# Kernel optimization log

Measured on AMD Instinct MI355X. Metric: run time of the kernel, lower is better.

The kernel has to match this reference:

```python
import jax, jax.numpy as jnp
import numpy as np

D_MODEL = 1024
N_HEAD = 16
HEAD_DIM = D_MODEL // N_HEAD
BS, SEQ = 4, 2048
NEG_INF = -1e9


def setup_inputs() -> dict:
    key = jax.random.key(0)
    ks = jax.random.split(key, 10)
    X = jax.random.normal(ks[0], (BS, SEQ, D_MODEL), dtype=jnp.float32)
    kpm = jax.random.randint(ks[1], (BS, SEQ), 0, 2, dtype=jnp.int32)
    kpm = kpm.at[:, 0].set(0)  # guarantee at least one attendable key per batch
    scale = 1.0 / np.sqrt(D_MODEL)
    WQ = jax.random.normal(ks[2], (D_MODEL, D_MODEL), dtype=jnp.float32) * scale
    bQ = jnp.zeros((D_MODEL,), dtype=jnp.float32)
    WK = jax.random.normal(ks[3], (D_MODEL, D_MODEL), dtype=jnp.float32) * scale
    bK = jnp.zeros((D_MODEL,), dtype=jnp.float32)
    WV = jax.random.normal(ks[4], (D_MODEL, D_MODEL), dtype=jnp.float32) * scale
    bV = jnp.zeros((D_MODEL,), dtype=jnp.float32)
    WO = jax.random.normal(ks[5], (D_MODEL, D_MODEL), dtype=jnp.float32) * scale
    bO = jnp.zeros((D_MODEL,), dtype=jnp.float32)
    return {"X": X, "key_padding_mask": kpm, "WQ": WQ, "bQ": bQ,
            "WK": WK, "bK": bK, "WV": WV, "bV": bV, "WO": WO, "bO": bO}


def reference(X, key_padding_mask, WQ, bQ, WK, bK, WV, bV, WO, bO):
    bs, L, _ = X.shape
    # separate Q/K/V linear projections (torch Linear: x @ W.T + b)
    Q = X @ WQ.T + bQ
    K = X @ WK.T + bK
    V = X @ WV.T + bV
    # split heads: (bs, L, H, Dh) -> (bs, H, L, Dh)
    Q = Q.reshape(bs, L, N_HEAD, HEAD_DIM).transpose(0, 2, 1, 3)
    K = K.reshape(bs, L, N_HEAD, HEAD_DIM).transpose(0, 2, 1, 3)
    V = V.reshape(bs, L, N_HEAD, HEAD_DIM).transpose(0, 2, 1, 3)
    # scaled dot-product attention
    scores = jnp.einsum('bhqd,bhkd->bhqk', Q, K) / jnp.sqrt(
        jnp.asarray(HEAD_DIM, dtype=Q.dtype))
    # key padding mask: non-zero => ignore that key
    mask = (key_padding_mask != 0)[:, None, None, :]  # (bs,1,1,L)
    scores = jnp.where(mask, NEG_INF, scores)
    attn = jax.nn.softmax(scores, axis=-1)
    out = jnp.einsum('bhqk,bhkd->bhqd', attn, V)
    # merge heads
    out = out.transpose(0, 2, 1, 3).reshape(bs, L, D_MODEL)
    return out @ WO.T + bO
```

## Files before the change

### kernel.cpp

```cpp
#include <hip/hip_runtime.h>
#include <stdint.h>

#define BS_   4
#define SEQ_  2048
#define DM_   1024
#define NH_   16
#define DH_   64
#define MTOK_ (BS_*SEQ_)

typedef __attribute__((ext_vector_type(8))) short bf16x8;
typedef __attribute__((ext_vector_type(4))) float f32x4;

#define SA_ 0.18033688011112042f
#define SHIFT_ 16.0f

__device__ __forceinline__ unsigned short f2bf(float f) {
    union { float f; uint32_t u; } v; v.f = f;
    uint32_t r = v.u + 0x7fffu + ((v.u >> 16) & 1u);
    return (unsigned short)(r >> 16);
}

__device__ __forceinline__ float fexp2(float x) {
#if __has_builtin(__builtin_amdgcn_exp2f)
    return __builtin_amdgcn_exp2f(x);
#else
    return __expf(x * 0.69314718055994531f);
#endif
}

__device__ __forceinline__ uint32_t cvt_pk_bf16(float lo, float hi) {
    uint32_t r;
    asm("v_cvt_pk_bf16_f32 %0, %1, %2" : "=v"(r) : "v"(lo), "v"(hi));
    return r;
}

__device__ __forceinline__ void gload_lds16(const void* g, void* l) {
    __builtin_amdgcn_global_load_lds(
        (const __attribute__((address_space(1))) void*)g,
        (__attribute__((address_space(3))) void*)l, 16, 0, 0);
}

__global__ void cvt_kernel(const float* __restrict__ src,
                           unsigned short* __restrict__ dst, int n) {
    int i = (blockIdx.x * blockDim.x + threadIdx.x) * 4;
    const int stride = gridDim.x * blockDim.x * 4;
    for (; i < n; i += stride) {
        float4 v = *(const float4*)(src + i);
        ushort4 o;
        o.x = f2bf(v.x); o.y = f2bf(v.y); o.z = f2bf(v.z); o.w = f2bf(v.w);
        *(ushort4*)(dst + i) = o;
    }
}

__global__ void cvt4_kernel(const float* __restrict__ s0, const float* __restrict__ s1,
                            const float* __restrict__ s2, const float* __restrict__ s3,
                            unsigned short* __restrict__ dst) {
    const int i = (blockIdx.x * blockDim.x + threadIdx.x) * 4;
    const int mat = i >> 20;
    const int off = i & ((1 << 20) - 1);
    const float* s = (mat == 0) ? s0 : (mat == 1) ? s1 : (mat == 2) ? s2 : s3;
    float4 v = *(const float4*)(s + off);
    ushort4 o;
    o.x = f2bf(v.x); o.y = f2bf(v.y); o.z = f2bf(v.z); o.w = f2bf(v.w);
    *(ushort4*)(dst + i) = o;
}

template<int MODE>
__global__ __launch_bounds__(256) void gemm_bt(
    const unsigned short* __restrict__ A,
    const unsigned short* __restrict__ B,
    int Ndim, int Kdim,
    const float* __restrict__ bias0,
    const float* __restrict__ bias1,
    const float* __restrict__ bias2,
    unsigned short* __restrict__ Qo,
    unsigned short* __restrict__ Ko,
    unsigned short* __restrict__ Vt,
    float* __restrict__ Co)
{
    __shared__ unsigned short As[128 * 32];
    __shared__ unsigned short Bs[128 * 32];

    const int t    = threadIdx.x;
    const int lane = t & 63;
    const int w    = t >> 6;
    const int wr   = w >> 1, wc = w & 1;
    const int g    = lane >> 4, li = lane & 15;

    const int ntile = Ndim >> 7;
    const int per   = gridDim.x >> 3;
    const int sw    = (blockIdx.x & 7) * per + (blockIdx.x >> 3);
    const int tm = sw / ntile;
    const int tn = sw % ntile;

    const unsigned short* Ab = A + (size_t)tm * 128 * Kdim;
    const unsigned short* Bb = B + (size_t)tn * 128 * Kdim;

    f32x4 acc[4][4];
    const f32x4 zero = {0.f, 0.f, 0.f, 0.f};
    #pragma unroll
    for (int i = 0; i < 4; ++i)
        #pragma unroll
        for (int j = 0; j < 4; ++j)
            acc[i][j] = zero;

    const int s0 = t, s1 = t + 256;
    const int r0 = s0 >> 2, c0 = (s0 & 3) << 3;
    const int r1 = s1 >> 2, c1 = (s1 & 3) << 3;

    for (int k0 = 0; k0 < Kdim; k0 += 32) {
        gload_lds16(Ab + (size_t)r0 * Kdim + k0 + c0, (char*)As + s0 * 16);
        gload_lds16(Ab + (size_t)r1 * Kdim + k0 + c1, (char*)As + s1 * 16);
        gload_lds16(Bb + (size_t)r0 * Kdim + k0 + c0, (char*)Bs + s0 * 16);
        gload_lds16(Bb + (size_t)r1 * Kdim + k0 + c1, (char*)Bs + s1 * 16);
        __syncthreads();

        bf16x8 a[4], b[4];
        #pragma unroll
        for (int mi = 0; mi < 4; ++mi)
            a[mi] = *(const bf16x8*)&As[(wr * 64 + mi * 16 + li) * 32 + g * 8];
        #pragma unroll
        for (int ni = 0; ni < 4; ++ni)
            b[ni] = *(const bf16x8*)&Bs[(wc * 64 + ni * 16 + li) * 32 + g * 8];

        #pragma unroll
        for (int mi = 0; mi < 4; ++mi)
            #pragma unroll
            for (int ni = 0; ni < 4; ++ni)
                acc[mi][ni] = __builtin_amdgcn_mfma_f32_16x16x32_bf16(
                    a[mi], b[ni], acc[mi][ni], 0, 0, 0);
        __syncthreads();
    }

    if constexpr (MODE == 0) {
        #pragma unroll
        for (int mi = 0; mi < 4; ++mi) {
            const int gm0 = tm * 128 + wr * 64 + mi * 16 + g * 4;
            const int bb  = gm0 >> 11;
            const int l0  = gm0 & (SEQ_ - 1);
            #pragma unroll
            for (int ni = 0; ni < 4; ++ni) {
                const int gn  = tn * 128 + wc * 64 + ni * 16 + li;
                const int mat = gn >> 10;
                const int c   = gn & (DM_ - 1);
                const int hh  = c >> 6;
                const int dd  = c & (DH_ - 1);
                const float bias = (mat == 0 ? bias0 : (mat == 1 ? bias1 : bias2))[c];
                const f32x4 v = acc[mi][ni];
                if (mat == 2) {
                    ushort4 o;
                    o.x = f2bf(v[0] + bias);
                    o.y = f2bf(v[1] + bias);
                    o.z = f2bf(v[2] + bias);
                    o.w = f2bf(v[3] + bias);
                    *(ushort4*)&Vt[((size_t)(bb * NH_ + hh) * DH_ + dd) * SEQ_ + l0] = o;
                } else {
                    unsigned short* dst = (mat == 0) ? Qo : Ko;
                    #pragma unroll
                    for (int r = 0; r < 4; ++r)
                        dst[((size_t)(bb * NH_ + hh) * SEQ_ + l0 + r) * DH_ + dd] =
                            f2bf(v[r] + bias);
                }
            }
        }
    } else {
        #pragma unroll
        for (int mi = 0; mi < 4; ++mi) {
            const int gm0 = tm * 128 + wr * 64 + mi * 16 + g * 4;
            #pragma unroll
            for (int ni = 0; ni < 4; ++ni) {
                const int gn = tn * 128 + wc * 64 + ni * 16 + li;
                const float bias = bias0[gn];
                #pragma unroll
                for (int r = 0; r < 4; ++r)
                    Co[(size_t)(gm0 + r) * Ndim + gn] = acc[mi][ni][r] + bias;
            }
        }
    }
}

#define KPAD 72

__global__ __launch_bounds__(256) void attn_kernel(
    const unsigned short* __restrict__ Q,
    const unsigned short* __restrict__ K,
    const unsigned short* __restrict__ Vt,
    const int* __restrict__ kpm,
    unsigned short* __restrict__ Oo)
{
    __shared__ unsigned short Ks[64 * KPAD];
    __shared__ unsigned short Vs[64 * KPAD];
    __shared__ float maskLds[64];

    const int t    = threadIdx.x;
    const int lane = t & 63;
    const int w    = t >> 6;
    const int g    = lane >> 4, li = lane & 15;

    const int bh = blockIdx.x >> 4;
    const int qt = blockIdx.x & 15;
    const int b  = bh >> 4;
    const int h  = bh & 15;
    const int q0 = qt * 128 + w * 32;

    bf16x8 qf[2][2];
    #pragma unroll
    for (int qi = 0; qi < 2; ++qi)
        #pragma unroll
        for (int kk = 0; kk < 2; ++kk)
            qf[qi][kk] = *(const bf16x8*)&Q[((size_t)bh * SEQ_ + q0 + qi * 16 + li) * DH_
                                            + kk * 32 + g * 8];

    f32x4 Oacc[2][4];
    const f32x4 zero = {0.f, 0.f, 0.f, 0.f};
    #pragma unroll
    for (int qi = 0; qi < 2; ++qi)
        #pragma unroll
        for (int di = 0; di < 4; ++di)
            Oacc[qi][di] = zero;

    float lrun[2] = {0.f, 0.f};

    const int sr = t >> 3;
    const int sc = (t & 7) * 8;

    bf16x8 kreg0, kreg1, vreg0, vreg1;
    float mreg = 0.f;

    auto load_tile = [&](int kv) {
        kreg0 = *(const bf16x8*)&K[((size_t)bh * SEQ_ + kv + sr) * DH_ + sc];
        kreg1 = *(const bf16x8*)&K[((size_t)bh * SEQ_ + kv + sr + 32) * DH_ + sc];
        vreg0 = *(const bf16x8*)&Vt[((size_t)bh * DH_ + sr) * SEQ_ + kv + sc];
        vreg1 = *(const bf16x8*)&Vt[((size_t)bh * DH_ + sr + 32) * SEQ_ + kv + sc];
        if (t < 64) mreg = (kpm[b * SEQ_ + kv + t] ? -1e9f : 0.0f) - SHIFT_;
    };
    auto store_tile = [&]() {
        *(bf16x8*)&Ks[sr * KPAD + sc] = kreg0;
        *(bf16x8*)&Ks[(sr + 32) * KPAD + sc] = kreg1;
        *(bf16x8*)&Vs[sr * KPAD + sc] = vreg0;
        *(bf16x8*)&Vs[(sr + 32) * KPAD + sc] = vreg1;
        if (t < 64) maskLds[t] = mreg;
    };

    load_tile(0);
    store_tile();

    for (int kv = 0; kv < SEQ_; kv += 64) {
        __syncthreads();
        const bool more = (kv + 64) < SEQ_;
        if (more) load_tile(kv + 64);

        float4 mk[4];
        #pragma unroll
        for (int ni = 0; ni < 4; ++ni)
            mk[ni] = *(const float4*)&maskLds[ni * 16 + g * 4];

        f32x4 sacc[2][4];
        #pragma unroll
        for (int qi = 0; qi < 2; ++qi)
            #pragma unroll
            for (int ni = 0; ni < 4; ++ni)
                sacc[qi][ni] = zero;
        __builtin_amdgcn_s_setprio(1);
        #pragma unroll
        for (int ni = 0; ni < 4; ++ni) {
            #pragma unroll
            for (int kk = 0; kk < 2; ++kk) {
                bf16x8 kb = *(const bf16x8*)&Ks[(ni * 16 + li) * KPAD + kk * 32 + g * 8];
                sacc[0][ni] = __builtin_amdgcn_mfma_f32_16x16x32_bf16(
                    kb, qf[0][kk], sacc[0][ni], 0, 0, 0);
                sacc[1][ni] = __builtin_amdgcn_mfma_f32_16x16x32_bf16(
                    kb, qf[1][kk], sacc[1][ni], 0, 0, 0);
            }
        }
        __builtin_amdgcn_s_setprio(0);

        #pragma unroll
        for (int qi = 0; qi < 2; ++qi) {
            float rs = 0.f;
            #pragma unroll
            for (int ni = 0; ni < 4; ++ni) {
                #pragma unroll
                for (int r = 0; r < 4; ++r) {
                    const float mval = (r == 0) ? mk[ni].x : (r == 1) ? mk[ni].y
                                      : (r == 2) ? mk[ni].z : mk[ni].w;
                    const float p = fexp2(fmaf(sacc[qi][ni][r], SA_, mval));
                    sacc[qi][ni][r] = p;
                    rs += p;
                }
            }
            lrun[qi] += rs;
        }

        bf16x8 pa[2][2];
        #pragma unroll
        for (int qi = 0; qi < 2; ++qi)
            #pragma unroll
            for (int kk = 0; kk < 2; ++kk) {
                union { bf16x8 v; uint32_t w4[4]; } u;
                u.w4[0] = cvt_pk_bf16(sacc[qi][2 * kk][0],     sacc[qi][2 * kk][1]);
                u.w4[1] = cvt_pk_bf16(sacc[qi][2 * kk][2],     sacc[qi][2 * kk][3]);
                u.w4[2] = cvt_pk_bf16(sacc[qi][2 * kk + 1][0], sacc[qi][2 * kk + 1][1]);
                u.w4[3] = cvt_pk_bf16(sacc[qi][2 * kk + 1][2], sacc[qi][2 * kk + 1][3]);
                pa[qi][kk] = u.v;
            }

        __builtin_amdgcn_s_setprio(1);
        #pragma unroll
        for (int di = 0; di < 4; ++di) {
            #pragma unroll
            for (int kk = 0; kk < 2; ++kk) {
                union { bf16x8 v; ushort4 h[2]; } uv;
                uv.h[0] = *(const ushort4*)&Vs[(di * 16 + li) * KPAD + kk * 32 + g * 4];
                uv.h[1] = *(const ushort4*)&Vs[(di * 16 + li) * KPAD + kk * 32 + 16 + g * 4];
                Oacc[0][di] = __builtin_amdgcn_mfma_f32_16x16x32_bf16(
                    uv.v, pa[0][kk], Oacc[0][di], 0, 0, 0);
                Oacc[1][di] = __builtin_amdgcn_mfma_f32_16x16x32_bf16(
                    uv.v, pa[1][kk], Oacc[1][di], 0, 0, 0);
            }
        }
        __builtin_amdgcn_s_setprio(0);

        __syncthreads();
        if (more) store_tile();
    }

    #pragma unroll
    for (int qi = 0; qi < 2; ++qi) {
        float lt = lrun[qi];
        lt += __shfl_xor(lt, 16);
        lt += __shfl_xor(lt, 32);
        const float inv = 1.0f / lt;
        const int q = q0 + qi * 16 + li;
        #pragma unroll
        for (int di = 0; di < 4; ++di) {
            ushort4 o;
            o.x = f2bf(Oacc[qi][di][0] * inv);
            o.y = f2bf(Oacc[qi][di][1] * inv);
            o.z = f2bf(Oacc[qi][di][2] * inv);
            o.w = f2bf(Oacc[qi][di][3] * inv);
            *(ushort4*)&Oo[((size_t)b * SEQ_ + q) * DM_ + h * 64 + di * 16 + g * 4] = o;
        }
    }
}

extern "C" void kernel_launch(void* const* d_in, const int* in_sizes, int n_in,
                              void* d_out, int out_size, void* d_ws, size_t ws_size,
                              hipStream_t stream) {
    const float* X  = (const float*)d_in[0];
    const int*  kpm = (const int*)d_in[1];
    const float* WQ = (const float*)d_in[2];
    const float* bQ = (const float*)d_in[3];
    const float* WK = (const float*)d_in[4];
    const float* bK = (const float*)d_in[5];
    const float* WV = (const float*)d_in[6];
    const float* bV = (const float*)d_in[7];
    const float* WO = (const float*)d_in[8];
    const float* bO = (const float*)d_in[9];
    float* Out = (float*)d_out;

    char* ws = (char*)d_ws;
    unsigned short* Xb  = (unsigned short*)(ws);
    unsigned short* Wb  = (unsigned short*)(ws + (16u << 20));
    unsigned short* WOb = (unsigned short*)(ws + (22u << 20));
    unsigned short* Qb  = (unsigned short*)(ws + (24u << 20));
    unsigned short* Kb  = (unsigned short*)(ws + (40u << 20));
    unsigned short* Vtb = (unsigned short*)(ws + (56u << 20));
    unsigned short* AOb = Xb;

    cvt_kernel<<<2048, 256, 0, stream>>>(X, Xb, (int)(MTOK_ * DM_));
    cvt4_kernel<<<4096, 256, 0, stream>>>(WQ, WK, WV, WO, Wb);

    gemm_bt<0><<<(MTOK_ / 128) * (3 * DM_ / 128), 256, 0, stream>>>(
        Xb, Wb, 3 * DM_, DM_, bQ, bK, bV, Qb, Kb, Vtb, nullptr);

    attn_kernel<<<BS_ * NH_ * (SEQ_ / 128), 256, 0, stream>>>(Qb, Kb, Vtb, kpm, AOb);

    gemm_bt<1><<<(MTOK_ / 128) * (DM_ / 128), 256, 0, stream>>>(
        AOb, WOb, DM_, DM_, bO, nullptr, nullptr, nullptr, nullptr, nullptr, Out);
}
```

Baseline: 227.4 us.

## Double-buffer K/V tiles in LDS and compute softmax row sums via MFMA

Doubles the K, V and mask LDS buffers so the next tile is stored into the alternate buffer, which removes the second __syncthreads per iteration. It also drops the per-element scalar accumulation of the softmax denominator and instead gets the row sums from an extra MFMA against a ones fragment, using the bf16-rounded probabilities. This cuts barrier stalls and VALU adds in exchange for more LDS per block (possible occupancy loss) and four extra MFMAs per tile.

```diff
diff --git a/kernel.cpp b/kernel.cpp
--- a/kernel.cpp
+++ b/kernel.cpp
@@ -188,9 +188,9 @@
     const int* __restrict__ kpm,
     unsigned short* __restrict__ Oo)
 {
-    __shared__ unsigned short Ks[64 * KPAD];
-    __shared__ unsigned short Vs[64 * KPAD];
-    __shared__ float maskLds[64];
+    __shared__ unsigned short Ks[2][64 * KPAD];
+    __shared__ unsigned short Vs[2][64 * KPAD];
+    __shared__ float maskLds[2][64];
 
     const int t    = threadIdx.x;
     const int lane = t & 63;
@@ -211,15 +211,23 @@
             qf[qi][kk] = *(const bf16x8*)&Q[((size_t)bh * SEQ_ + q0 + qi * 16 + li) * DH_
                                             + kk * 32 + g * 8];
 
+    bf16x8 ones_frag;
+    {
+        const short ob = (li == 0) ? (short)0x3F80 : (short)0;
+        #pragma unroll
+        for (int j = 0; j < 8; ++j) ones_frag[j] = ob;
+    }
+
     f32x4 Oacc[2][4];
+    f32x4 Lacc[2];
     const f32x4 zero = {0.f, 0.f, 0.f, 0.f};
     #pragma unroll
-    for (int qi = 0; qi < 2; ++qi)
+    for (int qi = 0; qi < 2; ++qi) {
+        Lacc[qi] = zero;
         #pragma unroll
         for (int di = 0; di < 4; ++di)
             Oacc[qi][di] = zero;
-
-    float lrun[2] = {0.f, 0.f};
+    }
 
     const int sr = t >> 3;
     const int sc = (t & 7) * 8;
@@ -234,17 +242,18 @@
         vreg1 = *(const bf16x8*)&Vt[((size_t)bh * DH_ + sr + 32) * SEQ_ + kv + sc];
         if (t < 64) mreg = (kpm[b * SEQ_ + kv + t] ? -1e9f : 0.0f) - SHIFT_;
     };
-    auto store_tile = [&]() {
-        *(bf16x8*)&Ks[sr * KPAD + sc] = kreg0;
-        *(bf16x8*)&Ks[(sr + 32) * KPAD + sc] = kreg1;
-        *(bf16x8*)&Vs[sr * KPAD + sc] = vreg0;
-        *(bf16x8*)&Vs[(sr + 32) * KPAD + sc] = vreg1;
-        if (t < 64) maskLds[t] = mreg;
+    auto store_tile = [&](int buf) {
+        *(bf16x8*)&Ks[buf][sr * KPAD + sc] = kreg0;
+        *(bf16x8*)&Ks[buf][(sr + 32) * KPAD + sc] = kreg1;
+        *(bf16x8*)&Vs[buf][sr * KPAD + sc] = vreg0;
+        *(bf16x8*)&Vs[buf][(sr + 32) * KPAD + sc] = vreg1;
+        if (t < 64) maskLds[buf][t] = mreg;
     };
 
     load_tile(0);
-    store_tile();
-
+    store_tile(0);
+
+    int cur = 0;
     for (int kv = 0; kv < SEQ_; kv += 64) {
         __syncthreads();
         const bool more = (kv + 64) < SEQ_;
@@ -253,7 +262,7 @@
         float4 mk[4];
         #pragma unroll
         for (int ni = 0; ni < 4; ++ni)
-            mk[ni] = *(const float4*)&maskLds[ni * 16 + g * 4];
+            mk[ni] = *(const float4*)&maskLds[cur][ni * 16 + g * 4];
 
         f32x4 sacc[2][4];
         #pragma unroll
@@ -266,7 +275,7 @@
         for (int ni = 0; ni < 4; ++ni) {
             #pragma unroll
             for (int kk = 0; kk < 2; ++kk) {
-                bf16x8 kb = *(const bf16x8*)&Ks[(ni * 16 + li) * KPAD + kk * 32 + g * 8];
+                bf16x8 kb = *(const bf16x8*)&Ks[cur][(ni * 16 + li) * KPAD + kk * 32 + g * 8];
                 sacc[0][ni] = __builtin_amdgcn_mfma_f32_16x16x32_bf16(
                     kb, qf[0][kk], sacc[0][ni], 0, 0, 0);
                 sacc[1][ni] = __builtin_amdgcn_mfma_f32_16x16x32_bf16(
@@ -277,19 +286,15 @@
 
         #pragma unroll
         for (int qi = 0; qi < 2; ++qi) {
-            float rs = 0.f;
             #pragma unroll
             for (int ni = 0; ni < 4; ++ni) {
                 #pragma unroll
                 for (int r = 0; r < 4; ++r) {
                     const float mval = (r == 0) ? mk[ni].x : (r == 1) ? mk[ni].y
                                       : (r == 2) ? mk[ni].z : mk[ni].w;
-                    const float p = fexp2(fmaf(sacc[qi][ni][r], SA_, mval));
-                    sacc[qi][ni][r] = p;
-                    rs += p;
+                    sacc[qi][ni][r] = fexp2(fmaf(sacc[qi][ni][r], SA_, mval));
                 }
             }
-            lrun[qi] += rs;
         }
 
         bf16x8 pa[2][2];
@@ -310,26 +315,30 @@
         for (int di = 0; di < 4; ++di) {
             #pragma unroll
             for (int kk = 0; kk < 2; ++kk) {
-                union { bf16x8 v; ushort4 h[2]; } uv;
-                uv.h[0] = *(const ushort4*)&Vs[(di * 16 + li) * KPAD + kk * 32 + g * 4];
-                uv.h[1] = *(const ushort4*)&Vs[(di * 16 + li) * KPAD + kk * 32 + 16 + g * 4];
+                union { bf16x8 v; ushort4 hh[2]; } uv;
+                uv.hh[0] = *(const ushort4*)&Vs[cur][(di * 16 + li) * KPAD + kk * 32 + g * 4];
+                uv.hh[1] = *(const ushort4*)&Vs[cur][(di * 16 + li) * KPAD + kk * 32 + 16 + g * 4];
                 Oacc[0][di] = __builtin_amdgcn_mfma_f32_16x16x32_bf16(
                     uv.v, pa[0][kk], Oacc[0][di], 0, 0, 0);
                 Oacc[1][di] = __builtin_amdgcn_mfma_f32_16x16x32_bf16(
                     uv.v, pa[1][kk], Oacc[1][di], 0, 0, 0);
             }
         }
+        #pragma unroll
+        for (int qi = 0; qi < 2; ++qi)
+            #pragma unroll
+            for (int kk = 0; kk < 2; ++kk)
+                Lacc[qi] = __builtin_amdgcn_mfma_f32_16x16x32_bf16(
+                    ones_frag, pa[qi][kk], Lacc[qi], 0, 0, 0);
         __builtin_amdgcn_s_setprio(0);
 
-        __syncthreads();
-        if (more) store_tile();
+        if (more) store_tile(cur ^ 1);
+        cur ^= 1;
     }
 
     #pragma unroll
     for (int qi = 0; qi < 2; ++qi) {
-        float lt = lrun[qi];
-        lt += __shfl_xor(lt, 16);
-        lt += __shfl_xor(lt, 32);
+        const float lt = __shfl(Lacc[qi][0], li);
         const float inv = 1.0f / lt;
         const int q = q0 + qi * 16 + li;
         #pragma unroll
```

New measurement: 230.9 us. About the same (+1.5%).
